# Kernel optimization log

Measured on AMD Instinct MI355X. Metric: run time of the kernel, lower is better.

## Reference

```python
import jax, jax.numpy as jnp
import numpy as np

BS, SL, D, NH = 2, 2048, 1024, 16
HD = D // NH
SCALE = D ** (-0.5)  # NOTE: source scales by full model dim, not head dim


def setup_inputs() -> dict:
    key = jax.random.key(0)
    k1, k2, k3 = jax.random.split(key, 3)
    return {
        "input_sequence": jax.random.normal(k1, (BS, SL, D), dtype=jnp.float32),
        "w_qkv": jax.random.normal(k2, (D, 3 * D), dtype=jnp.float32) * (D ** -0.5),
        "w_out": jax.random.normal(k3, (D, D), dtype=jnp.float32) * (D ** -0.5),
    }


def reference(input_sequence, w_qkv, w_out):
    bs, sl, od = input_sequence.shape
    nh, hd = NH, od // NH
    qkv = input_sequence @ w_qkv                      # [bs, sl, 3d]
    q, k, v = jnp.split(qkv, 3, axis=-1)              # each [bs, sl, d]
    q = q * SCALE

    def heads(x):  # [bs, sl, d] -> [bs, nh, sl, hd]
        return x.reshape(bs, sl, nh, hd).transpose(0, 2, 1, 3)

    q, k, v = heads(q), heads(k), heads(v)
    scores = jnp.einsum("bhqd,bhkd->bhqk", q, k)      # [bs, nh, sl, sl]
    weights = jax.nn.softmax(scores, axis=-1)
    ctx = jnp.einsum("bhqk,bhkd->bhqd", weights, v)   # [bs, nh, sl, hd]
    ctx = ctx.transpose(0, 2, 1, 3).reshape(bs, sl, od)
    return ctx @ w_out
```

## Files before the change

kernel.cpp:

```cpp
#include <hip/hip_runtime.h>
#include <cstdint>
#include <cstddef>

typedef float f32x4 __attribute__((ext_vector_type(4)));
typedef float f32x16 __attribute__((ext_vector_type(16)));
typedef __bf16 bf16x8 __attribute__((ext_vector_type(8)));
typedef __bf16 bf16x4 __attribute__((ext_vector_type(4)));
typedef uint32_t u32x4 __attribute__((ext_vector_type(4)));

static constexpr int BSZ = 2, SL = 2048, DM = 1024, NH = 16, HD = 64;
static constexpr int MROWS = BSZ * SL;
static constexpr float LOG2E = 1.4426950408889634f;
static constexpr float QSCALE = 0.03125f * LOG2E;

__device__ __forceinline__ f32x4 mfma16(bf16x8 a, bf16x8 b, f32x4 c) {
    return __builtin_amdgcn_mfma_f32_16x16x32_bf16(a, b, c, 0, 0, 0);
}
__device__ __forceinline__ f32x16 mfma32(bf16x8 a, bf16x8 b, f32x16 c) {
    return __builtin_amdgcn_mfma_f32_32x32x16_bf16(a, b, c, 0, 0, 0);
}
__device__ __forceinline__ uint32_t pkbf(float lo, float hi) {
    uint16_t a = __builtin_bit_cast(uint16_t, (__bf16)lo);
    uint16_t b = __builtin_bit_cast(uint16_t, (__bf16)hi);
    return ((uint32_t)b << 16) | (uint32_t)a;
}

__global__ __launch_bounds__(256) void r6_cast(const float* __restrict__ in,
                                               __bf16* __restrict__ out, int n) {
    int i = (blockIdx.x * 256 + threadIdx.x) * 4;
    if (i >= n) return;
    float4 v = *(const float4*)&in[i];
    bf16x4 o;
    o.x = (__bf16)v.x; o.y = (__bf16)v.y; o.z = (__bf16)v.z; o.w = (__bf16)v.w;
    *(bf16x4*)&out[i] = o;
}

__global__ __launch_bounds__(256) void r6_transpose_cast(const float* __restrict__ in,
                                                         __bf16* __restrict__ out,
                                                         int R, int C) {
    __shared__ float tile[32][33];
    int c0 = blockIdx.x * 32, r0 = blockIdx.y * 32;
    int tx = threadIdx.x & 31, ty = threadIdx.x >> 5;
#pragma unroll
    for (int i = 0; i < 32; i += 8)
        tile[ty + i][tx] = in[(size_t)(r0 + ty + i) * C + c0 + tx];
    __syncthreads();
#pragma unroll
    for (int i = 0; i < 32; i += 8)
        out[(size_t)(c0 + ty + i) * R + r0 + tx] = (__bf16)tile[tx][ty + i];
}

template <int EPI>
__global__ __launch_bounds__(256) void r6_gemm_bt(
    const __bf16* __restrict__ A, const __bf16* __restrict__ Bt,
    float* __restrict__ ob, int M, int N, int K,
    __bf16* __restrict__ qb, __bf16* __restrict__ kb, __bf16* __restrict__ vtb)
{
    constexpr int BM = 128, BN = 128, BK = 32, LDP = 40;
    __shared__ __bf16 As[BM][LDP];
    __shared__ __bf16 Bs[BN][LDP];
    const int tid  = threadIdx.x;
    const int m0   = blockIdx.y * BM, n0 = blockIdx.x * BN;
    const int wave = tid >> 6, lane = tid & 63;
    const int lcol = lane & 15, lgrp = lane >> 4;
    const int wm   = (wave >> 1) * 64, wn = (wave & 1) * 64;

    f32x4 acc[4][4] = {};

    for (int k0 = 0; k0 < K; k0 += BK) {
#pragma unroll
        for (int i = 0; i < 2; ++i) {
            int c = tid + 256 * i;
            int row = c >> 2, off = (c & 3) * 8;
            *(int4*)&As[row][off] = *(const int4*)&A[(size_t)(m0 + row) * K + k0 + off];
            *(int4*)&Bs[row][off] = *(const int4*)&Bt[(size_t)(n0 + row) * K + k0 + off];
        }
        __syncthreads();
        bf16x8 af[4], bfr[4];
#pragma unroll
        for (int f = 0; f < 4; ++f) {
            af[f]  = *(const bf16x8*)&As[wm + f * 16 + lcol][lgrp * 8];
            bfr[f] = *(const bf16x8*)&Bs[wn + f * 16 + lcol][lgrp * 8];
        }
#pragma unroll
        for (int fm = 0; fm < 4; ++fm)
#pragma unroll
            for (int fn = 0; fn < 4; ++fn)
                acc[fm][fn] = mfma16(af[fm], bfr[fn], acc[fm][fn]);
        __syncthreads();
    }

#pragma unroll
    for (int fm = 0; fm < 4; ++fm) {
#pragma unroll
        for (int fn = 0; fn < 4; ++fn) {
            int n = n0 + wn + fn * 16 + lcol;
#pragma unroll
            for (int r = 0; r < 4; ++r) {
                int m = m0 + wm + fm * 16 + lgrp * 4 + r;
                float v = acc[fm][fn][r];
                if (EPI == 0) {
                    ob[(size_t)m * N + n] = v;
                } else {
                    int sec = n >> 10, nm = n & 1023;
                    int h = nm >> 6, d = nm & 63;
                    int b = m >> 11, s = m & 2047;
                    size_t bh = (size_t)(b * NH + h);
                    if (sec == 0)      qb[(bh * SL + s) * HD + d]  = (__bf16)(v * QSCALE);
                    else if (sec == 1) kb[(bh * SL + s) * HD + d]  = (__bf16)v;
                    else               vtb[(bh * HD + d) * SL + s] = (__bf16)v;
                }
            }
        }
    }
}

#define PV_STEP(a0,a1,a2,a3,a4,a5,a6,a7, KS) do {                               \
    uint32_t w0 = pkbf(a0, a1), w1 = pkbf(a2, a3);                              \
    uint32_t w2 = pkbf(a4, a5), w3 = pkbf(a6, a7);                              \
    asm volatile("v_permlane32_swap_b32 %0, %1" : "+v"(w0), "+v"(w2));          \
    asm volatile("v_permlane32_swap_b32 %0, %1" : "+v"(w1), "+v"(w3));          \
    u32x4 pw = {w0, w1, w2, w3};                                                \
    bf16x8 pf = __builtin_bit_cast(bf16x8, pw);                                 \
    const int cv = (((KS) * 2 + h) ^ swz8) * 8;                                 \
    bf16x8 vf0 = *(const bf16x8*)&Vl[lq * 64 + cv];                             \
    bf16x8 vf1 = *(const bf16x8*)&Vl[(lq + 32) * 64 + cv];                      \
    accT0 = mfma32(vf0, pf, accT0);                                             \
    accT1 = mfma32(vf1, pf, accT1);                                             \
} while (0)

__global__ __launch_bounds__(256) void r6_attn(
    const __bf16* __restrict__ qb, const __bf16* __restrict__ kb,
    const __bf16* __restrict__ vtb, __bf16* __restrict__ ctx)
{
    __shared__ __bf16 KV[2][2][4096];
    __shared__ __bf16 Os[4][32][72];
    const int bh   = blockIdx.y;
    const int tid  = threadIdx.x;
    const int wave = tid >> 6, lane = tid & 63;
    const int lq = lane & 31, h = lane >> 5;
    const int swz8 = lq & 7;
    const int q0 = blockIdx.x * 128 + wave * 32;

    const __bf16* Q  = qb  + ((size_t)bh * SL + q0) * HD;
    const __bf16* Kg = kb  + (size_t)bh * SL * HD;
    const __bf16* Vg = vtb + (size_t)bh * HD * SL;

    const int rA = tid >> 3, cA = tid & 7;
    const int sA = cA ^ (rA & 7);
    const int oA = rA * 64 + sA * 8;

    bf16x8 qf[4];
#pragma unroll
    for (int t = 0; t < 4; ++t)
        qf[t] = *(const bf16x8*)&Q[(size_t)lq * HD + t * 16 + h * 8];

    f32x16 accT0 = {}, accT1 = {};
    float m_run = -1e30f, l_run = 0.f;

    const __bf16* KgA = Kg + rA * HD + cA * 8;
    const __bf16* VgA = Vg + (size_t)rA * SL + cA * 8;
    int4 kA = *(const int4*)(KgA);
    int4 kB = *(const int4*)(KgA + (size_t)32 * HD);
    int4 vA = *(const int4*)(VgA);
    int4 vB = *(const int4*)(VgA + (size_t)32 * SL);

    for (int t = 0; t < SL / 64; ++t) {
        const int cur = t & 1;
        {
            __bf16* dK = &KV[cur][0][oA];
            __bf16* dV = &KV[cur][1][oA];
            *(int4*)dK = kA;  *(int4*)(dK + 2048) = kB;
            *(int4*)dV = vA;  *(int4*)(dV + 2048) = vB;
        }
        if (t + 1 < SL / 64) {
            const __bf16* nK = KgA + (size_t)(t + 1) * 64 * HD;
            const __bf16* nV = VgA + (size_t)(t + 1) * 64;
            kA = *(const int4*)(nK);
            kB = *(const int4*)(nK + (size_t)32 * HD);
            vA = *(const int4*)(nV);
            vB = *(const int4*)(nV + (size_t)32 * SL);
        }
        __syncthreads();

        const __bf16* Kl = &KV[cur][0][0];
        const __bf16* Vl = &KV[cur][1][0];

        f32x16 s0 = {}, s1 = {};
        __builtin_amdgcn_s_setprio(1);
#pragma unroll
        for (int t4 = 0; t4 < 4; ++t4) {
            const int cv = ((t4 * 2 + h) ^ swz8) * 8;
            bf16x8 kf0 = *(const bf16x8*)&Kl[lq * 64 + cv];
            bf16x8 kf1 = *(const bf16x8*)&Kl[(lq + 32) * 64 + cv];
            s0 = mfma32(kf0, qf[t4], s0);
            s1 = mfma32(kf1, qf[t4], s1);
        }
        __builtin_amdgcn_s_setprio(0);

        float t16[16];
#pragma unroll
        for (int i = 0; i < 16; ++i) t16[i] = fmaxf(s0[i], s1[i]);
#pragma unroll
        for (int i = 0; i < 8; ++i) t16[i] = fmaxf(t16[i], t16[i + 8]);
#pragma unroll
        for (int i = 0; i < 4; ++i) t16[i] = fmaxf(t16[i], t16[i + 4]);
        float mt = fmaxf(fmaxf(t16[0], t16[1]), fmaxf(t16[2], t16[3]));
        mt = fmaxf(mt, __shfl_xor(mt, 32));
        if (__any(mt > m_run + 8.f)) {
            float mn = fmaxf(m_run, mt);
            float alpha = exp2f(m_run - mn);
            m_run = mn;
            l_run *= alpha;
            accT0 *= alpha;
            accT1 *= alpha;
        }
        float p0[16], p1[16];
#pragma unroll
        for (int i = 0; i < 16; ++i) {
            p0[i] = exp2f(s0[i] - m_run);
            p1[i] = exp2f(s1[i] - m_run);
        }
        float a16[16];
#pragma unroll
        for (int i = 0; i < 16; ++i) a16[i] = p0[i] + p1[i];
#pragma unroll
        for (int i = 0; i < 8; ++i) a16[i] += a16[i + 8];
#pragma unroll
        for (int i = 0; i < 4; ++i) a16[i] += a16[i + 4];
        float lt = (a16[0] + a16[1]) + (a16[2] + a16[3]);
        lt += __shfl_xor(lt, 32);
        l_run += lt;

        __builtin_amdgcn_s_setprio(1);
        PV_STEP(p0[0], p0[1], p0[2], p0[3], p0[4], p0[5], p0[6], p0[7], 0);
        PV_STEP(p0[8], p0[9], p0[10], p0[11], p0[12], p0[13], p0[14], p0[15], 1);
        PV_STEP(p1[0], p1[1], p1[2], p1[3], p1[4], p1[5], p1[6], p1[7], 2);
        PV_STEP(p1[8], p1[9], p1[10], p1[11], p1[12], p1[13], p1[14], p1[15], 3);
        __builtin_amdgcn_s_setprio(0);
    }

    float inv = 1.f / l_run;
#pragma unroll
    for (int r = 0; r < 16; ++r) {
        int d0 = (r & 3) + 8 * (r >> 2) + 4 * h;
        Os[wave][lq][d0]      = (__bf16)(accT0[r] * inv);
        Os[wave][lq][32 + d0] = (__bf16)(accT1[r] * inv);
    }
    asm volatile("s_waitcnt lgkmcnt(0)" ::: "memory");
    __builtin_amdgcn_sched_barrier(0);
    const int b = bh >> 4, head = bh & 15;
    const int qr = lane >> 1, seg = (lane & 1) * 32;
    __bf16* dst = &ctx[((size_t)b * SL + q0 + qr) * DM + head * HD + seg];
#pragma unroll
    for (int c = 0; c < 4; ++c)
        *(bf16x8*)&dst[c * 8] = *(const bf16x8*)&Os[wave][qr][seg + c * 8];
}

extern "C" void kernel_launch(void* const* d_in, const int* in_sizes, int n_in,
                              void* d_out, int out_size, void* d_ws, size_t ws_size,
                              hipStream_t stream) {
    const float* x    = (const float*)d_in[0];
    const float* wqkv = (const float*)d_in[1];
    const float* wout = (const float*)d_in[2];
    float* out = (float*)d_out;

    __bf16* ws    = (__bf16*)d_ws;
    __bf16* xb    = ws;
    __bf16* wqkvT = xb    + (size_t)MROWS * DM;
    __bf16* woutT = wqkvT + (size_t)3 * DM * DM;
    __bf16* qbuf  = woutT + (size_t)DM * DM;
    __bf16* kbuf  = qbuf  + (size_t)MROWS * DM;
    __bf16* vtbuf = kbuf  + (size_t)MROWS * DM;
    __bf16* ctxb  = vtbuf + (size_t)MROWS * DM;

    r6_cast<<<dim3((MROWS * DM) / 1024), dim3(256), 0, stream>>>(x, xb, MROWS * DM);
    r6_transpose_cast<<<dim3(96, 32), dim3(256), 0, stream>>>(wqkv, wqkvT, DM, 3 * DM);
    r6_transpose_cast<<<dim3(32, 32), dim3(256), 0, stream>>>(wout, woutT, DM, DM);

    r6_gemm_bt<1><<<dim3(24, 32), dim3(256), 0, stream>>>(
        xb, wqkvT, (float*)nullptr, MROWS, 3 * DM, DM, qbuf, kbuf, vtbuf);

    r6_attn<<<dim3(16, 32), dim3(256), 0, stream>>>(qbuf, kbuf, vtbuf, ctxb);

    r6_gemm_bt<0><<<dim3(8, 32), dim3(256), 0, stream>>>(
        ctxb, woutT, out, MROWS, DM, DM,
        (__bf16*)nullptr, (__bf16*)nullptr, (__bf16*)nullptr);
}
```

Measured before the change: 158.4 us.

## Split attention KV across two blocks with merge; async LDS loads in GEMM

Attention is split along the key/value dimension into two halves (grid z=2). Each half writes a partial normalized context plus a log-sum-exp value, and a new merge kernel combines the two halves. This doubles the attention grid from 512 to 1024 blocks to fill more CUs. The GEMMs now use global_load_lds direct-to-LDS loads with an unpadded layout, and the output projection uses BN=64 for more blocks. The cost is an extra merge pass, extra memory traffic for the partials, and possible LDS bank conflicts from the unpadded layout.

```diff
diff --git a/kernel.cpp b/kernel.cpp
--- a/kernel.cpp
+++ b/kernel.cpp
@@ -24,8 +24,13 @@
     uint16_t b = __builtin_bit_cast(uint16_t, (__bf16)hi);
     return ((uint32_t)b << 16) | (uint32_t)a;
 }
-
-__global__ __launch_bounds__(256) void r6_cast(const float* __restrict__ in,
+__device__ __forceinline__ void gload16(const void* g, void* l) {
+    __builtin_amdgcn_global_load_lds(
+        (const __attribute__((address_space(1))) uint32_t*)g,
+        (__attribute__((address_space(3))) uint32_t*)l, 16, 0, 0);
+}
+
+__global__ __launch_bounds__(256) void r7_cast(const float* __restrict__ in,
                                                __bf16* __restrict__ out, int n) {
     int i = (blockIdx.x * 256 + threadIdx.x) * 4;
     if (i >= n) return;
@@ -35,7 +40,7 @@
     *(bf16x4*)&out[i] = o;
 }
 
-__global__ __launch_bounds__(256) void r6_transpose_cast(const float* __restrict__ in,
+__global__ __launch_bounds__(256) void r7_transpose_cast(const float* __restrict__ in,
                                                          __bf16* __restrict__ out,
                                                          int R, int C) {
     __shared__ float tile[32][33];
@@ -50,42 +55,49 @@
         out[(size_t)(c0 + ty + i) * R + r0 + tx] = (__bf16)tile[tx][ty + i];
 }
 
-template <int EPI>
-__global__ __launch_bounds__(256) void r6_gemm_bt(
+template <int EPI, int BN>
+__global__ __launch_bounds__(256) void r7_gemm(
     const __bf16* __restrict__ A, const __bf16* __restrict__ Bt,
     float* __restrict__ ob, int M, int N, int K,
     __bf16* __restrict__ qb, __bf16* __restrict__ kb, __bf16* __restrict__ vtb)
 {
-    constexpr int BM = 128, BN = 128, BK = 32, LDP = 40;
-    __shared__ __bf16 As[BM][LDP];
-    __shared__ __bf16 Bs[BN][LDP];
+    constexpr int BM = 128, BK = 32;
+    constexpr int FN = BN / 32;
+    __shared__ __bf16 As[BM * BK];
+    __shared__ __bf16 Bs[BN * BK];
     const int tid  = threadIdx.x;
     const int m0   = blockIdx.y * BM, n0 = blockIdx.x * BN;
     const int wave = tid >> 6, lane = tid & 63;
     const int lcol = lane & 15, lgrp = lane >> 4;
-    const int wm   = (wave >> 1) * 64, wn = (wave & 1) * 64;
-
-    f32x4 acc[4][4] = {};
+    const int wm   = (wave >> 1) * 64, wn = (wave & 1) * (BN / 2);
+    const int grow = lane >> 2, gcol = (lane & 3) * 8;
+
+    f32x4 acc[4][FN] = {};
 
     for (int k0 = 0; k0 < K; k0 += BK) {
-#pragma unroll
-        for (int i = 0; i < 2; ++i) {
-            int c = tid + 256 * i;
-            int row = c >> 2, off = (c & 3) * 8;
-            *(int4*)&As[row][off] = *(const int4*)&A[(size_t)(m0 + row) * K + k0 + off];
-            *(int4*)&Bs[row][off] = *(const int4*)&Bt[(size_t)(n0 + row) * K + k0 + off];
+        {
+            const int cA0 = 2 * wave;
+            gload16(&A[(size_t)(m0 + cA0 * 16 + grow) * K + k0 + gcol], &As[cA0 * 512]);
+            gload16(&A[(size_t)(m0 + (cA0 + 1) * 16 + grow) * K + k0 + gcol], &As[(cA0 + 1) * 512]);
+            if constexpr (BN == 128) {
+                gload16(&Bt[(size_t)(n0 + cA0 * 16 + grow) * K + k0 + gcol], &Bs[cA0 * 512]);
+                gload16(&Bt[(size_t)(n0 + (cA0 + 1) * 16 + grow) * K + k0 + gcol], &Bs[(cA0 + 1) * 512]);
+            } else {
+                gload16(&Bt[(size_t)(n0 + wave * 16 + grow) * K + k0 + gcol], &Bs[wave * 512]);
+            }
         }
         __syncthreads();
-        bf16x8 af[4], bfr[4];
-#pragma unroll
-        for (int f = 0; f < 4; ++f) {
-            af[f]  = *(const bf16x8*)&As[wm + f * 16 + lcol][lgrp * 8];
-            bfr[f] = *(const bf16x8*)&Bs[wn + f * 16 + lcol][lgrp * 8];
-        }
+        bf16x8 af[4], bfr[FN];
+#pragma unroll
+        for (int f = 0; f < 4; ++f)
+            af[f] = *(const bf16x8*)&As[(wm + f * 16 + lcol) * BK + lgrp * 8];
+#pragma unroll
+        for (int f = 0; f < FN; ++f)
+            bfr[f] = *(const bf16x8*)&Bs[(wn + f * 16 + lcol) * BK + lgrp * 8];
 #pragma unroll
         for (int fm = 0; fm < 4; ++fm)
 #pragma unroll
-            for (int fn = 0; fn < 4; ++fn)
+            for (int fn = 0; fn < FN; ++fn)
                 acc[fm][fn] = mfma16(af[fm], bfr[fn], acc[fm][fn]);
         __syncthreads();
     }
@@ -93,7 +105,7 @@
 #pragma unroll
     for (int fm = 0; fm < 4; ++fm) {
 #pragma unroll
-        for (int fn = 0; fn < 4; ++fn) {
+        for (int fn = 0; fn < FN; ++fn) {
             int n = n0 + wn + fn * 16 + lcol;
 #pragma unroll
             for (int r = 0; r < 4; ++r) {
@@ -129,18 +141,20 @@
     accT1 = mfma32(vf1, pf, accT1);                                             \
 } while (0)
 
-__global__ __launch_bounds__(256) void r6_attn(
+__global__ __launch_bounds__(256) void r7_attn(
     const __bf16* __restrict__ qb, const __bf16* __restrict__ kb,
-    const __bf16* __restrict__ vtb, __bf16* __restrict__ ctx)
+    const __bf16* __restrict__ vtb, __bf16* __restrict__ part0,
+    __bf16* __restrict__ part1, float* __restrict__ ml)
 {
-    __shared__ __bf16 KV[2][2][4096];
-    __shared__ __bf16 Os[4][32][72];
-    const int bh   = blockIdx.y;
-    const int tid  = threadIdx.x;
-    const int wave = tid >> 6, lane = tid & 63;
+    __shared__ __bf16 arena[16384];
+    const int bh    = blockIdx.y;
+    const int split = blockIdx.z;
+    const int tid   = threadIdx.x;
+    const int wave  = tid >> 6, lane = tid & 63;
     const int lq = lane & 31, h = lane >> 5;
     const int swz8 = lq & 7;
     const int q0 = blockIdx.x * 128 + wave * 32;
+    const int kv0 = split * (SL / 2);
 
     const __bf16* Q  = qb  + ((size_t)bh * SL + q0) * HD;
     const __bf16* Kg = kb  + (size_t)bh * SL * HD;
@@ -158,22 +172,23 @@
     f32x16 accT0 = {}, accT1 = {};
     float m_run = -1e30f, l_run = 0.f;
 
-    const __bf16* KgA = Kg + rA * HD + cA * 8;
-    const __bf16* VgA = Vg + (size_t)rA * SL + cA * 8;
+    const __bf16* KgA = Kg + (size_t)(kv0 + rA) * HD + cA * 8;
+    const __bf16* VgA = Vg + (size_t)rA * SL + kv0 + cA * 8;
     int4 kA = *(const int4*)(KgA);
     int4 kB = *(const int4*)(KgA + (size_t)32 * HD);
     int4 vA = *(const int4*)(VgA);
     int4 vB = *(const int4*)(VgA + (size_t)32 * SL);
 
-    for (int t = 0; t < SL / 64; ++t) {
+    constexpr int NT = SL / 2 / 64;
+    for (int t = 0; t < NT; ++t) {
         const int cur = t & 1;
         {
-            __bf16* dK = &KV[cur][0][oA];
-            __bf16* dV = &KV[cur][1][oA];
+            __bf16* dK = &arena[cur * 8192 + oA];
+            __bf16* dV = dK + 4096;
             *(int4*)dK = kA;  *(int4*)(dK + 2048) = kB;
             *(int4*)dV = vA;  *(int4*)(dV + 2048) = vB;
         }
-        if (t + 1 < SL / 64) {
+        if (t + 1 < NT) {
             const __bf16* nK = KgA + (size_t)(t + 1) * 64 * HD;
             const __bf16* nV = VgA + (size_t)(t + 1) * 64;
             kA = *(const int4*)(nK);
@@ -183,8 +198,8 @@
         }
         __syncthreads();
 
-        const __bf16* Kl = &KV[cur][0][0];
-        const __bf16* Vl = &KV[cur][1][0];
+        const __bf16* Kl = &arena[cur * 8192];
+        const __bf16* Vl = Kl + 4096;
 
         f32x16 s0 = {}, s1 = {};
         __builtin_amdgcn_s_setprio(1);
@@ -240,21 +255,50 @@
         __builtin_amdgcn_s_setprio(0);
     }
 
+    if (h == 0)
+        ml[split * (32 * SL) + bh * SL + q0 + lq] = m_run + __log2f(l_run);
+
+    __syncthreads();
+    __bf16* Osw = &arena[wave * 2304];
     float inv = 1.f / l_run;
 #pragma unroll
     for (int r = 0; r < 16; ++r) {
         int d0 = (r & 3) + 8 * (r >> 2) + 4 * h;
-        Os[wave][lq][d0]      = (__bf16)(accT0[r] * inv);
-        Os[wave][lq][32 + d0] = (__bf16)(accT1[r] * inv);
+        Osw[lq * 72 + d0]      = (__bf16)(accT0[r] * inv);
+        Osw[lq * 72 + 32 + d0] = (__bf16)(accT1[r] * inv);
     }
     asm volatile("s_waitcnt lgkmcnt(0)" ::: "memory");
     __builtin_amdgcn_sched_barrier(0);
     const int b = bh >> 4, head = bh & 15;
     const int qr = lane >> 1, seg = (lane & 1) * 32;
-    __bf16* dst = &ctx[((size_t)b * SL + q0 + qr) * DM + head * HD + seg];
+    __bf16* pbase = split == 0 ? part0 : part1;
+    __bf16* dst = &pbase[((size_t)b * SL + q0 + qr) * DM + head * HD + seg];
 #pragma unroll
     for (int c = 0; c < 4; ++c)
-        *(bf16x8*)&dst[c * 8] = *(const bf16x8*)&Os[wave][qr][seg + c * 8];
+        *(bf16x8*)&dst[c * 8] = *(const bf16x8*)&Osw[qr * 72 + seg + c * 8];
+}
+
+__global__ __launch_bounds__(256) void r7_merge(
+    const __bf16* __restrict__ p0, const __bf16* __restrict__ p1,
+    const float* __restrict__ ml, __bf16* __restrict__ out)
+{
+    int idx = blockIdx.x * 256 + threadIdx.x;
+    int m = idx >> 7, g = idx & 127;
+    int d0 = g * 8, h = d0 >> 6;
+    int b = m >> 11, q = m & 2047;
+    int bhq = (b * NH + h) * SL + q;
+    float ml0 = ml[bhq], ml1 = ml[32 * SL + bhq];
+    float M = fmaxf(ml0, ml1);
+    float w0 = exp2f(ml0 - M), w1 = exp2f(ml1 - M);
+    float inv = 1.f / (w0 + w1);
+    w0 *= inv; w1 *= inv;
+    size_t off = (size_t)m * DM + d0;
+    bf16x8 a = *(const bf16x8*)&p0[off];
+    bf16x8 c = *(const bf16x8*)&p1[off];
+    bf16x8 o;
+#pragma unroll
+    for (int j = 0; j < 8; ++j) o[j] = (__bf16)(w0 * (float)a[j] + w1 * (float)c[j]);
+    *(bf16x8*)&out[off] = o;
 }
 
 extern "C" void kernel_launch(void* const* d_in, const int* in_sizes, int n_in,
@@ -273,17 +317,23 @@
     __bf16* kbuf  = qbuf  + (size_t)MROWS * DM;
     __bf16* vtbuf = kbuf  + (size_t)MROWS * DM;
     __bf16* ctxb  = vtbuf + (size_t)MROWS * DM;
-
-    r6_cast<<<dim3((MROWS * DM) / 1024), dim3(256), 0, stream>>>(x, xb, MROWS * DM);
-    r6_transpose_cast<<<dim3(96, 32), dim3(256), 0, stream>>>(wqkv, wqkvT, DM, 3 * DM);
-    r6_transpose_cast<<<dim3(32, 32), dim3(256), 0, stream>>>(wout, woutT, DM, DM);
-
-    r6_gemm_bt<1><<<dim3(24, 32), dim3(256), 0, stream>>>(
+    __bf16* part0 = xb;
+    __bf16* part1 = ctxb;
+    float*  mlbuf = (float*)wqkvT;
+
+    r7_cast<<<dim3((MROWS * DM) / 1024), dim3(256), 0, stream>>>(x, xb, MROWS * DM);
+    r7_transpose_cast<<<dim3(96, 32), dim3(256), 0, stream>>>(wqkv, wqkvT, DM, 3 * DM);
+    r7_transpose_cast<<<dim3(32, 32), dim3(256), 0, stream>>>(wout, woutT, DM, DM);
+
+    r7_gemm<1, 128><<<dim3(24, 32), dim3(256), 0, stream>>>(
         xb, wqkvT, (float*)nullptr, MROWS, 3 * DM, DM, qbuf, kbuf, vtbuf);
 
-    r6_attn<<<dim3(16, 32), dim3(256), 0, stream>>>(qbuf, kbuf, vtbuf, ctxb);
-
-    r6_gemm_bt<0><<<dim3(8, 32), dim3(256), 0, stream>>>(
+    r7_attn<<<dim3(16, 32, 2), dim3(256), 0, stream>>>(
+        qbuf, kbuf, vtbuf, part0, part1, mlbuf);
+
+    r7_merge<<<dim3(2048), dim3(256), 0, stream>>>(part0, part1, mlbuf, ctxb);
+
+    r7_gemm<0, 64><<<dim3(16, 32), dim3(256), 0, stream>>>(
         ctxb, woutT, out, MROWS, DM, DM,
         (__bf16*)nullptr, (__bf16*)nullptr, (__bf16*)nullptr);
 }
```

Measured after the change: 160.3 us. No clear change (+1.2%).
